# Optimization experiments

Measured on AMD Instinct MI355X. Metric: run time of the kernel, lower is better.

## Reference

```python
import jax, jax.numpy as jnp
import numpy as np

B, N, D, H, P, C, L = 2, 768, 512, 8, 64, 256, 6
NSEQ, NSP, NRD = 8, 8, 16
K = 2 * NSEQ + NSP + NRD  # 40 sparse neighbor slots
DH = D // H
LAT = 8


def _ln(x):
    m = jnp.mean(x, axis=-1, keepdims=True)
    v = jnp.var(x, axis=-1, keepdims=True)
    return (x - m) * jax.lax.rsqrt(v + 1e-5)


def _neighbors(ca, mask, rand_idx):
    # sequential neighbors: +-NSEQ offsets, clipped, with in-range validity
    offs = jnp.concatenate([jnp.arange(-NSEQ, 0), jnp.arange(1, NSEQ + 1)])
    base = jnp.arange(N)[:, None] + offs[None, :]                 # [N, 2*NSEQ]
    seq_idx = jnp.broadcast_to(jnp.clip(base, 0, N - 1)[None], (B, N, 2 * NSEQ))
    seq_in = jnp.broadcast_to(((base >= 0) & (base < N))[None], (B, N, 2 * NSEQ))
    # spatial KNN on CA coordinates (mask invalid residues and self)
    d2 = jnp.sum((ca[:, :, None, :] - ca[:, None, :, :]) ** 2, axis=-1)  # [B,N,N]
    big = jnp.float32(1e9)
    d2 = jnp.where(mask[:, None, :], d2, big)
    d2 = d2 + jnp.eye(N, dtype=d2.dtype) * big
    _, sp_idx = jax.lax.top_k(-d2, NSP)                            # [B,N,NSP]
    idx = jnp.concatenate([seq_idx.astype(jnp.int32), sp_idx.astype(jnp.int32),
                           rand_idx.astype(jnp.int32)], axis=-1)   # [B,N,K]
    b_ar = jnp.arange(B)[:, None, None]
    nb_mask = mask[b_ar, idx]                                      # neighbor validity
    extra = jnp.concatenate([seq_in, jnp.ones((B, N, NSP + NRD), bool)], axis=-1)
    valid = nb_mask & extra & mask[:, :, None]                     # [B,N,K]
    return idx, valid


def setup_inputs() -> dict:
    key = jax.random.key(0)
    ks = jax.random.split(key, 16)
    s = 0.02
    return {
        'seqs': jax.random.normal(ks[0], (B, N, D), jnp.float32),
        'cond': jax.random.normal(ks[1], (B, N, C), jnp.float32),
        'ca_coors': jax.random.normal(ks[2], (B, N, 3), jnp.float32) * 10.0,
        'pair_rep': jax.random.normal(ks[3], (B, N, N, P), jnp.float32),
        'mask': jnp.ones((B, N), bool),
        'rand_idx': jax.random.randint(ks[4], (B, N, NRD), 0, N, jnp.int32),
        'Wq': jax.random.normal(ks[5], (L, D, D), jnp.float32) * s,
        'Wk': jax.random.normal(ks[6], (L, D, D), jnp.float32) * s,
        'Wv': jax.random.normal(ks[7], (L, D, D), jnp.float32) * s,
        'Wo': jax.random.normal(ks[8], (L, D, D), jnp.float32) * s,
        'Wb': jax.random.normal(ks[9], (L, P, H), jnp.float32) * s,
        'Wc': jax.random.normal(ks[10], (L, C, 2 * D), jnp.float32) * s,
        'W1': jax.random.normal(ks[11], (L, D, 4 * D), jnp.float32) * s,
        'W2': jax.random.normal(ks[12], (L, 4 * D, D), jnp.float32) * s,
        'W_ca': jax.random.normal(ks[13], (D, 3), jnp.float32) * s,
        'W_lat': jax.random.normal(ks[14], (D, LAT), jnp.float32) * s,
    }


def reference(seqs, cond, ca_coors, pair_rep, mask, rand_idx,
              Wq, Wk, Wv, Wo, Wb, Wc, W1, W2, W_ca, W_lat):
    idx, valid = _neighbors(ca_coors, mask, rand_idx)              # [B,N,K]
    b_ar = jnp.arange(B)[:, None, None]
    # gather pair features once for all layers: [B,N,K,P]
    pair_g = jnp.take_along_axis(pair_rep, idx[:, :, :, None], axis=2)
    scale = 1.0 / jnp.sqrt(jnp.float32(DH))
    mview = mask[:, :, None].astype(seqs.dtype)
    x = seqs
    for l in range(L):
        h = _ln(x)
        ss = cond @ Wc[l]                                          # adaLN-style cond
        sc, sh = jnp.split(ss, 2, axis=-1)
        h = h * (1.0 + sc) + sh
        q = (h @ Wq[l]).reshape(B, N, H, DH)
        k_all = h @ Wk[l]
        v_all = h @ Wv[l]
        kg = k_all[b_ar, idx].reshape(B, N, K, H, DH)              # sparse gather
        vg = v_all[b_ar, idx].reshape(B, N, K, H, DH)
        q = _ln(q)                                                 # qk-layernorm
        kg = _ln(kg)
        bias = jnp.einsum('bnkp,ph->bhnk', pair_g, Wb[l])          # pair bias
        scores = jnp.einsum('bnhd,bnkhd->bhnk', q, kg) * scale + bias
        scores = jnp.where(valid[:, None, :, :], scores, -1e9)
        attn = jax.nn.softmax(scores, axis=-1)
        o = jnp.einsum('bhnk,bnkhd->bnhd', attn, vg).reshape(B, N, D)
        x = x + (o @ Wo[l]) * mview
        t = jax.nn.gelu(_ln(x) @ W1[l]) @ W2[l]                    # transition MLP
        x = x + t * mview
    hN = _ln(x)
    ca_out = hN @ W_ca                                             # [B,N,3]
    lat = hN @ W_lat                                               # [B,N,LAT]
    return jnp.concatenate([ca_out, lat], axis=-1)
```

## Files before the change

### kernel.cpp

```cpp
#include <hip/hip_runtime.h>
#include <hip/hip_bf16.h>


constexpr int B_  = 2;
constexpr int N_  = 768;
constexpr int D_  = 512;
constexpr int H_  = 8;
constexpr int P_  = 64;
constexpr int C_  = 256;
constexpr int L_  = 6;
constexpr int NSEQ = 8;
constexpr int NSP  = 8;
constexpr int NRD  = 16;
constexpr int K_   = 2 * NSEQ + NSP + NRD;
constexpr int DH_  = D_ / H_;
constexpr int BN_  = B_ * N_;
constexpr int D2_  = 2 * D_;
constexpr int D3_  = 3 * D_;
constexpr int D4_  = 4 * D_;

constexpr int FB_SS  = 0;
constexpr int FB_QKV = 512;
constexpr int FB_WO  = 2048;
constexpr int FB_W1  = 2560;
constexpr int FB_W2  = 4608;
constexpr int FB_TOT = 6656;

typedef __attribute__((ext_vector_type(8))) short bf16x8;
typedef __attribute__((ext_vector_type(4))) float floatx4;

__device__ __forceinline__ float waveRedSum(float v) {
#pragma unroll
    for (int o = 32; o > 0; o >>= 1) v += __shfl_xor(v, o, 64);
    return v;
}
__device__ __forceinline__ float waveRedMax(float v) {
#pragma unroll
    for (int o = 32; o > 0; o >>= 1) v = fmaxf(v, __shfl_xor(v, o, 64));
    return v;
}

__device__ __forceinline__ unsigned short bf_hi(float x) {
    unsigned u = __float_as_uint(x);
    return (unsigned short)((u + 0x7FFFu + ((u >> 16) & 1u)) >> 16);
}
__device__ __forceinline__ float bf_f(unsigned short h) {
    return __uint_as_float(((unsigned)h) << 16);
}
__device__ __forceinline__ void split2(float x0, float x1, unsigned& hp, unsigned& lp) {
    unsigned short h0 = bf_hi(x0), h1 = bf_hi(x1);
    unsigned short l0 = bf_hi(x0 - bf_f(h0)), l1 = bf_hi(x1 - bf_f(h1));
    hp = (unsigned)h0 | ((unsigned)h1 << 16);
    lp = (unsigned)l0 | ((unsigned)l1 << 16);
}

__device__ __forceinline__ float gelu_tanh(float x) {
    float u = x * x * x;
    float z = 0.7978845608028654f * (x + 0.044715f * u);
    float az = fabsf(z);
    float e = __expf(-2.f * az);
    float th = (1.f - e) / (1.f + e);
    th = (z < 0.f) ? -th : th;
    return 0.5f * x * (1.f + th);
}

__global__ void copy_kernel(const float4* __restrict__ in, float4* __restrict__ out, int n4) {
    int i = blockIdx.x * 256 + threadIdx.x;
    if (i < n4) out[i] = in[i];
}

__global__ __launch_bounds__(256) void knn_kernel(const float* __restrict__ ca,
                                                  const int* __restrict__ rnd,
                                                  int* __restrict__ idx) {
    __shared__ float sx[N_], sy[N_], sz[N_];
    __shared__ float cv[4];
    __shared__ int   ci[4];
    int bn = blockIdx.x;
    int b = bn / N_, n = bn % N_;
    int t = threadIdx.x;
    int wid = t >> 6, lane = t & 63;
    const float* cab = ca + (size_t)b * N_ * 3;
    for (int j = t; j < N_; j += 256) {
        sx[j] = cab[j * 3 + 0];
        sy[j] = cab[j * 3 + 1];
        sz[j] = cab[j * 3 + 2];
    }
    __syncthreads();
    float ax = sx[n], ay = sy[n], az = sz[n];

    float d2l[3];
    int   jls[3];
#pragma unroll
    for (int r = 0; r < 3; ++r) {
        int j = t + r * 256;
        float dx = ax - sx[j], dy = ay - sy[j], dz = az - sz[j];
        float d2 = dx * dx + dy * dy + dz * dz;
        if (j == n) d2 += 1e9f;
        d2l[r] = d2;
        jls[r] = j;
    }

    int base = bn * K_;
    if (t < 2 * NSEQ) {
        int off = (t < NSEQ) ? (t - NSEQ) : (t - NSEQ + 1);
        int p = n + off;
        p = p < 0 ? 0 : (p > N_ - 1 ? N_ - 1 : p);
        idx[base + t] = p;
    }
    if (t < NRD) idx[base + 2 * NSEQ + NSP + t] = rnd[bn * NRD + t];

    bool taken[3] = {false, false, false};
    for (int s = 0; s < NSP; ++s) {
        float bv = 3.4e38f;
        int   bi = N_;
#pragma unroll
        for (int r = 0; r < 3; ++r) {
            if (!taken[r]) {
                float v = d2l[r];
                if (v < bv || (v == bv && jls[r] < bi)) { bv = v; bi = jls[r]; }
            }
        }
#pragma unroll
        for (int o = 32; o > 0; o >>= 1) {
            float v2 = __shfl_xor(bv, o, 64);
            int   i2 = __shfl_xor(bi, o, 64);
            if (v2 < bv || (v2 == bv && i2 < bi)) { bv = v2; bi = i2; }
        }
        if (lane == 0) { cv[wid] = bv; ci[wid] = bi; }
        __syncthreads();
        float mv = cv[0]; int mi = ci[0];
#pragma unroll
        for (int w = 1; w < 4; ++w) {
            if (cv[w] < mv || (cv[w] == mv && ci[w] < mi)) { mv = cv[w]; mi = ci[w]; }
        }
        int sel = mi;
        if (t == 0) idx[base + 2 * NSEQ + s] = sel;
#pragma unroll
        for (int r = 0; r < 3; ++r)
            if (jls[r] == sel) taken[r] = true;
        __syncthreads();
    }
}

__global__ __launch_bounds__(256) void wconv_kernel(const float* __restrict__ Wc,
                                                    const float* __restrict__ Wq,
                                                    const float* __restrict__ Wk,
                                                    const float* __restrict__ Wv,
                                                    const float* __restrict__ Wo,
                                                    const float* __restrict__ W1,
                                                    const float* __restrict__ W2,
                                                    uint4* __restrict__ Wt, int l0) {
    int wid = threadIdx.x >> 6, lane = threadIdx.x & 63;
    int per = FB_TOT / 4;
    int slot = blockIdx.x / per;
    int l = l0 + slot;
    int fb = (blockIdx.x - slot * per) * 4 + wid;
    const float* src;
    int Nsrc, nsub, kstep;
    if (fb < FB_QKV) {
        int r = fb; nsub = r >> 3; kstep = r & 7;
        src = Wc + (size_t)l * C_ * D2_; Nsrc = D2_;
    } else if (fb < FB_WO) {
        int r = fb - FB_QKV; nsub = r >> 4; kstep = r & 15;
        int sel = nsub >> 5;
        const float* s0 = (sel == 0) ? Wq : ((sel == 1) ? Wk : Wv);
        src = s0 + (size_t)l * D_ * D_; Nsrc = D_; nsub &= 31;
    } else if (fb < FB_W1) {
        int r = fb - FB_WO; nsub = r >> 4; kstep = r & 15;
        src = Wo + (size_t)l * D_ * D_; Nsrc = D_;
    } else if (fb < FB_W2) {
        int r = fb - FB_W1; nsub = r >> 4; kstep = r & 15;
        src = W1 + (size_t)l * D_ * D4_; Nsrc = D4_;
    } else {
        int r = fb - FB_W2; nsub = r >> 6; kstep = r & 63;
        src = W2 + (size_t)l * D4_ * D_; Nsrc = D_;
    }
    int k0 = kstep * 32 + ((lane >> 4) << 3);
    int n = nsub * 16 + (lane & 15);
    unsigned hp[4], lp[4];
#pragma unroll
    for (int jj = 0; jj < 4; ++jj) {
        float x0 = src[(size_t)(k0 + 2 * jj) * Nsrc + n];
        float x1 = src[(size_t)(k0 + 2 * jj + 1) * Nsrc + n];
        split2(x0, x1, hp[jj], lp[jj]);
    }
    uint4* dst = Wt + ((size_t)slot * FB_TOT + fb) * 128;
    dst[lane]      = (uint4){hp[0], hp[1], hp[2], hp[3]};
    dst[64 + lane] = (uint4){lp[0], lp[1], lp[2], lp[3]};
}

__global__ __launch_bounds__(256) void pair_bias_kernel(const float* __restrict__ pair,
                                                        const float* __restrict__ WbL,
                                                        const int* __restrict__ idx,
                                                        float* __restrict__ biasL) {
    int wid = threadIdx.x >> 6, lane = threadIdx.x & 63;
    int t = blockIdx.x * 4 + wid;
    int bn = t / K_;
    int j = idx[t];
    float pv = pair[((size_t)bn * N_ + j) * P_ + lane];
    float4 wa = *(const float4*)&WbL[lane * 8];
    float4 wb = *(const float4*)&WbL[lane * 8 + 4];
    float r0 = waveRedSum(pv * wa.x);
    float r1 = waveRedSum(pv * wa.y);
    float r2 = waveRedSum(pv * wa.z);
    float r3 = waveRedSum(pv * wa.w);
    float r4 = waveRedSum(pv * wb.x);
    float r5 = waveRedSum(pv * wb.y);
    float r6 = waveRedSum(pv * wb.z);
    float r7 = waveRedSum(pv * wb.w);
    float res = r0;
    res = (lane == 1) ? r1 : res;
    res = (lane == 2) ? r2 : res;
    res = (lane == 3) ? r3 : res;
    res = (lane == 4) ? r4 : res;
    res = (lane == 5) ? r5 : res;
    res = (lane == 6) ? r6 : res;
    res = (lane == 7) ? r7 : res;
    if (lane < 8) biasL[(size_t)t * 8 + lane] = res;
}

#define STAGE_A(BUF)                                                        \
    {                                                                       \
        unsigned h0, h1, h2, h3, p0, p1, p2, p3;                            \
        split2(fa0.x, fa0.y, h0, p0); split2(fa0.z, fa0.w, h1, p1);         \
        split2(fa1.x, fa1.y, h2, p2); split2(fa1.z, fa1.w, h3, p3);         \
        As[BUF][sidx]      = (uint4){h0, h1, h2, h3};                       \
        As[BUF][64 + sidx] = (uint4){p0, p1, p2, p3};                       \
    }

#define MFMA_PHASE(BUF, BH, BL)                                             \
    {                                                                       \
        bf16x8 Ah[4], Al[4];                                                \
        _Pragma("unroll")                                                   \
        for (int mf = 0; mf < 4; ++mf) {                                    \
            Ah[mf] = *(const bf16x8*)&As[BUF][mf * 128 + lane];             \
            Al[mf] = *(const bf16x8*)&As[BUF][mf * 128 + 64 + lane];        \
        }                                                                   \
        _Pragma("unroll")                                                   \
        for (int mf = 0; mf < 4; ++mf) {                                    \
            _Pragma("unroll")                                               \
            for (int nf = 0; nf < 2; ++nf) {                                \
                acc[mf][nf] = __builtin_amdgcn_mfma_f32_16x16x32_bf16(      \
                    Ah[mf], BH[nf], acc[mf][nf], 0, 0, 0);                  \
                acc[mf][nf] = __builtin_amdgcn_mfma_f32_16x16x32_bf16(      \
                    Ah[mf], BL[nf], acc[mf][nf], 0, 0, 0);                  \
                acc[mf][nf] = __builtin_amdgcn_mfma_f32_16x16x32_bf16(      \
                    Al[mf], BH[nf], acc[mf][nf], 0, 0, 0);                  \
            }                                                               \
        }                                                                   \
    }

template <int GELU, int RES>
__global__ __launch_bounds__(256, 2) void gemm_mfma(const float* __restrict__ A,
                                                    const uint4* __restrict__ WtB,
                                                    const float* __restrict__ Cres,
                                                    float* __restrict__ Cout,
                                                    int M, int Nout, int Kd) {
    __shared__ uint4 As[2][512];
    int tid = threadIdx.x;
    int wid = tid >> 6, lane = tid & 63;
    int m0 = blockIdx.y * 64, n0 = blockIdx.x * 128;
    int kd32 = Kd >> 5;

    int sr = tid >> 2, soct = tid & 3;
    const float* Ap = A + (size_t)(m0 + sr) * Kd + soct * 8;
    int sidx = (sr >> 4) * 128 + (sr & 15) + soct * 16;

    int nsub0 = (n0 >> 4) + wid * 2;
    const uint4* Bp0 = WtB + (size_t)nsub0 * kd32 * 128 + lane;
    const uint4* Bp1 = WtB + (size_t)(nsub0 + 1) * kd32 * 128 + lane;

    floatx4 acc[4][2];
#pragma unroll
    for (int i = 0; i < 4; ++i)
#pragma unroll
        for (int j = 0; j < 2; ++j) acc[i][j] = (floatx4){0.f, 0.f, 0.f, 0.f};

    float4 fa0, fa1;
    bf16x8 BhA[2], BlA[2], BhB[2], BlB[2];

    fa0 = *(const float4*)(Ap);
    fa1 = *(const float4*)(Ap + 4);
    STAGE_A(0)
    BhA[0] = *(const bf16x8*)(Bp0);
    BlA[0] = *(const bf16x8*)(Bp0 + 64);
    BhA[1] = *(const bf16x8*)(Bp1);
    BlA[1] = *(const bf16x8*)(Bp1 + 64);
    __syncthreads();

    for (int ks = 0; ks < kd32; ks += 2) {
        fa0 = *(const float4*)(Ap + (ks + 1) * 32);
        fa1 = *(const float4*)(Ap + (ks + 1) * 32 + 4);
        BhB[0] = *(const bf16x8*)(Bp0 + (size_t)(ks + 1) * 128);
        BlB[0] = *(const bf16x8*)(Bp0 + (size_t)(ks + 1) * 128 + 64);
        BhB[1] = *(const bf16x8*)(Bp1 + (size_t)(ks + 1) * 128);
        BlB[1] = *(const bf16x8*)(Bp1 + (size_t)(ks + 1) * 128 + 64);
        MFMA_PHASE(0, BhA, BlA)
        STAGE_A(1)
        __syncthreads();

        bool more = (ks + 2) < kd32;
        if (more) {
            fa0 = *(const float4*)(Ap + (ks + 2) * 32);
            fa1 = *(const float4*)(Ap + (ks + 2) * 32 + 4);
            BhA[0] = *(const bf16x8*)(Bp0 + (size_t)(ks + 2) * 128);
            BlA[0] = *(const bf16x8*)(Bp0 + (size_t)(ks + 2) * 128 + 64);
            BhA[1] = *(const bf16x8*)(Bp1 + (size_t)(ks + 2) * 128);
            BlA[1] = *(const bf16x8*)(Bp1 + (size_t)(ks + 2) * 128 + 64);
        }
        MFMA_PHASE(1, BhB, BlB)
        if (more) STAGE_A(0)
        __syncthreads();
    }

    int r0 = (lane >> 4) << 2;
    int cc = lane & 15;
#pragma unroll
    for (int mf = 0; mf < 4; ++mf) {
#pragma unroll
        for (int nf = 0; nf < 2; ++nf) {
            int nn = n0 + (wid * 2 + nf) * 16 + cc;
#pragma unroll
            for (int r = 0; r < 4; ++r) {
                int mm = m0 + mf * 16 + r0 + r;
                float x = acc[mf][nf][r];
                if (GELU) x = gelu_tanh(x);
                if (RES) x += Cres[(size_t)mm * Nout + nn];
                Cout[(size_t)mm * Nout + nn] = x;
            }
        }
    }
}

template <bool MOD>
__global__ __launch_bounds__(256) void ln_kernel(const float* __restrict__ x,
                                                 const float* __restrict__ ss,
                                                 float* __restrict__ out) {
    __shared__ float sred[8];
    int row = blockIdx.x, t = threadIdx.x;
    int wid = t >> 6, lane = t & 63;
    const float* xr = x + (size_t)row * D_;
    float v0 = xr[t], v1 = xr[t + 256];
    float p = waveRedSum(v0 + v1);
    float q = waveRedSum(v0 * v0 + v1 * v1);
    if (lane == 0) { sred[wid] = p; sred[wid + 4] = q; }
    __syncthreads();
    float mean = (sred[0] + sred[1] + sred[2] + sred[3]) * (1.0f / D_);
    float var = (sred[4] + sred[5] + sred[6] + sred[7]) * (1.0f / D_) - mean * mean;
    float rs = rsqrtf(var + 1e-5f);
    float h0 = (v0 - mean) * rs;
    float h1 = (v1 - mean) * rs;
    if (MOD) {
        const float* ssr = ss + (size_t)row * D2_;
        h0 = h0 * (1.f + ssr[t]) + ssr[t + D_];
        h1 = h1 * (1.f + ssr[t + 256]) + ssr[t + 256 + D_];
    }
    float* orow = out + (size_t)row * D_;
    orow[t] = h0;
    orow[t + 256] = h1;
}

__global__ __launch_bounds__(256) void ln_head_kernel(float* __restrict__ qkv) {
    int wid = threadIdx.x >> 6, lane = threadIdx.x & 63;
    int vec = blockIdx.x * 4 + wid;
    int part = vec / (BN_ * H_);
    int rem = vec - part * (BN_ * H_);
    int r = rem / H_, h = rem - r * H_;
    float* p = qkv + (size_t)r * D3_ + part * D_ + h * DH_;
    float v = p[lane];
    float s = waveRedSum(v);
    float sq = waveRedSum(v * v);
    float m = s * (1.f / DH_);
    float var = sq * (1.f / DH_) - m * m;
    p[lane] = (v - m) * rsqrtf(var + 1e-5f);
}

__global__ __launch_bounds__(256) void attn_kernel(const float* __restrict__ qkv,
                                                   const int* __restrict__ idx,
                                                   const float* __restrict__ biasL,
                                                   float* __restrict__ o) {
    int wid = threadIdx.x >> 6, lane = threadIdx.x & 63;
    int g = blockIdx.x * 4 + wid;
    int h = g & 7;
    int bn = g >> 3;
    int n = bn % N_;
    int bnb = bn - n;

    int myj = 0;
    float mybias = 0.f;
    bool myvalid = false;
    if (lane < K_) {
        myj = idx[bn * K_ + lane];
        mybias = biasL[((size_t)bn * K_ + lane) * H_ + h];
        myvalid = true;
        if (lane < 2 * NSEQ) {
            int off = (lane < NSEQ) ? (lane - NSEQ) : (lane - NSEQ + 1);
            int p = n + off;
            myvalid = (p >= 0) && (p < N_);
        }
    }
    float qv = qkv[(size_t)bn * D3_ + h * DH_ + lane];
    float sc = -1e9f;
#pragma unroll 8
    for (int k = 0; k < K_; ++k) {
        int j = __shfl(myj, k);
        float kv = qkv[(size_t)(bnb + j) * D3_ + D_ + h * DH_ + lane];
        float dot = waveRedSum(qv * kv);
        if (lane == k) sc = myvalid ? (dot * 0.125f + mybias) : -1e9f;
    }
    float mx = waveRedMax(lane < K_ ? sc : -3.4e38f);
    float e = (lane < K_) ? expf(sc - mx) : 0.f;
    float den = waveRedSum(e);
    float w = e / den;
    float acc = 0.f;
#pragma unroll 8
    for (int k = 0; k < K_; ++k) {
        int j = __shfl(myj, k);
        float wk = __shfl(w, k);
        acc += wk * qkv[(size_t)(bnb + j) * D3_ + 2 * D_ + h * DH_ + lane];
    }
    o[(size_t)bn * D_ + h * DH_ + lane] = acc;
}

__global__ __launch_bounds__(256) void final_kernel(const float* __restrict__ x,
                                                    const float* __restrict__ Wca,
                                                    const float* __restrict__ Wlat,
                                                    float* __restrict__ out) {
    __shared__ float sred[8];
    __shared__ float hn[D_];
    int row = blockIdx.x, t = threadIdx.x;
    int wid = t >> 6, lane = t & 63;
    const float* xr = x + (size_t)row * D_;
    float v0 = xr[t], v1 = xr[t + 256];
    float p = waveRedSum(v0 + v1);
    float q = waveRedSum(v0 * v0 + v1 * v1);
    if (lane == 0) { sred[wid] = p; sred[wid + 4] = q; }
    __syncthreads();
    float mean = (sred[0] + sred[1] + sred[2] + sred[3]) * (1.0f / D_);
    float var = (sred[4] + sred[5] + sred[6] + sred[7]) * (1.0f / D_) - mean * mean;
    float rs = rsqrtf(var + 1e-5f);
    hn[t] = (v0 - mean) * rs;
    hn[t + 256] = (v1 - mean) * rs;
    __syncthreads();
    for (int c = wid; c < 11; c += 4) {
        float s = 0.f;
#pragma unroll
        for (int u = 0; u < 8; ++u) {
            int d = lane + u * 64;
            float w = (c < 3) ? Wca[d * 3 + c] : Wlat[d * 8 + (c - 3)];
            s += hn[d] * w;
        }
        s = waveRedSum(s);
        if (lane == 0) out[(size_t)row * 11 + c] = s;
    }
}

extern "C" void kernel_launch(void* const* d_in, const int* in_sizes, int n_in,
                              void* d_out, int out_size, void* d_ws, size_t ws_size,
                              hipStream_t stream) {
    const float* seqs = (const float*)d_in[0];
    const float* cond = (const float*)d_in[1];
    const float* ca   = (const float*)d_in[2];
    const float* pair = (const float*)d_in[3];
    const int*   rnd  = (const int*)d_in[5];
    const float* Wq   = (const float*)d_in[6];
    const float* Wk   = (const float*)d_in[7];
    const float* Wv   = (const float*)d_in[8];
    const float* Wo   = (const float*)d_in[9];
    const float* Wb   = (const float*)d_in[10];
    const float* Wc   = (const float*)d_in[11];
    const float* W1   = (const float*)d_in[12];
    const float* W2   = (const float*)d_in[13];
    const float* Wca  = (const float*)d_in[14];
    const float* Wlat = (const float*)d_in[15];
    float* out = (float*)d_out;

    const size_t wtSlotF = (size_t)FB_TOT * 512;
    const size_t fixedF = (size_t)BN_ * D_ * 3 + (size_t)BN_ * K_ * H_ + BN_ * K_
                        + (size_t)BN_ * D2_ + (size_t)BN_ * D3_;
    bool allW = ws_size >= (fixedF + (size_t)L_ * wtSlotF) * 4;
    int nslots = allW ? L_ : 1;

    float* ws = (float*)d_ws;
    float* x     = ws;  ws += BN_ * D_;
    float* hbuf  = ws;  ws += BN_ * D_;
    float* obuf  = ws;  ws += BN_ * D_;
    float* biasL = ws;  ws += BN_ * K_ * H_;
    int*   idx   = (int*)ws;  ws += BN_ * K_;
    uint4* Wt    = (uint4*)ws; ws += nslots * wtSlotF;
    float* ss    = ws;  ws += BN_ * D2_;
    float* qkv   = ws;  ws += BN_ * D3_;
    float* t1    = ss;

    copy_kernel<<<BN_ * D_ / 4 / 256, 256, 0, stream>>>((const float4*)seqs, (float4*)x, BN_ * D_ / 4);
    knn_kernel<<<BN_, 256, 0, stream>>>(ca, rnd, idx);
    if (allW)
        wconv_kernel<<<L_ * (FB_TOT / 4), 256, 0, stream>>>(Wc, Wq, Wk, Wv, Wo, W1, W2, Wt, 0);

    dim3 blk(256);
    for (int l = 0; l < L_; ++l) {
        if (!allW)
            wconv_kernel<<<FB_TOT / 4, 256, 0, stream>>>(Wc, Wq, Wk, Wv, Wo, W1, W2, Wt, l);
        const uint4* WtL = Wt + (size_t)(allW ? l : 0) * FB_TOT * 128;
        const float* WbL = Wb + (size_t)l * P_ * H_;

        pair_bias_kernel<<<BN_ * K_ / 4, blk, 0, stream>>>(pair, WbL, idx, biasL);
        gemm_mfma<0, 0><<<dim3(D2_ / 128, BN_ / 64), blk, 0, stream>>>(
            cond, WtL + (size_t)FB_SS * 128, nullptr, ss, BN_, D2_, C_);
        ln_kernel<true><<<BN_, blk, 0, stream>>>(x, ss, hbuf);
        gemm_mfma<0, 0><<<dim3(D3_ / 128, BN_ / 64), blk, 0, stream>>>(
            hbuf, WtL + (size_t)FB_QKV * 128, nullptr, qkv, BN_, D3_, D_);
        ln_head_kernel<<<BN_ * H_ * 2 / 4, blk, 0, stream>>>(qkv);
        attn_kernel<<<BN_ * H_ / 4, blk, 0, stream>>>(qkv, idx, biasL, obuf);
        gemm_mfma<0, 1><<<dim3(D_ / 128, BN_ / 64), blk, 0, stream>>>(
            obuf, WtL + (size_t)FB_WO * 128, x, x, BN_, D_, D_);
        ln_kernel<false><<<BN_, blk, 0, stream>>>(x, nullptr, hbuf);
        gemm_mfma<1, 0><<<dim3(D4_ / 128, BN_ / 64), blk, 0, stream>>>(
            hbuf, WtL + (size_t)FB_W1 * 128, nullptr, t1, BN_, D4_, D_);
        gemm_mfma<0, 1><<<dim3(D_ / 128, BN_ / 64), blk, 0, stream>>>(
            t1, WtL + (size_t)FB_W2 * 128, x, x, BN_, D_, D4_);
    }

    final_kernel<<<BN_, blk, 0, stream>>>(x, Wca, Wlat, out);
}
```

Measured before the change: 1.747 ms.

## Split-K residual GEMMs with atomics, fuse LN into W1 GEMM, hoist pair bias

Pair-bias computation for all layers is hoisted into one launch before the layer loop, so each gathered pair row is read once instead of once per layer. The Wo and W2 GEMMs are split two ways along K and accumulate into x with atomicAdd. This doubles their block count and replaces the explicit residual read. The plain LayerNorm before W1 becomes a small stats kernel, and normalization is applied while staging A tiles inside the GEMM, removing the hbuf write and read. GEMM blocks are also remapped with a swizzled 1D grid. Atomic accumulation makes the float summation order nondeterministic, and the full path needs more workspace.

```diff
diff --git a/kernel.cpp b/kernel.cpp
--- a/kernel.cpp
+++ b/kernel.cpp
@@ -18,6 +18,7 @@
 constexpr int D2_  = 2 * D_;
 constexpr int D3_  = 3 * D_;
 constexpr int D4_  = 4 * D_;
+constexpr int MROWS_ = BN_ / 64;
 
 constexpr int FB_SS  = 0;
 constexpr int FB_QKV = 512;
@@ -190,40 +191,69 @@
 }
 
 __global__ __launch_bounds__(256) void pair_bias_kernel(const float* __restrict__ pair,
-                                                        const float* __restrict__ WbL,
+                                                        const float* __restrict__ Wb,
                                                         const int* __restrict__ idx,
-                                                        float* __restrict__ biasL) {
+                                                        float* __restrict__ biasAll,
+                                                        int l0, int nl) {
     int wid = threadIdx.x >> 6, lane = threadIdx.x & 63;
     int t = blockIdx.x * 4 + wid;
     int bn = t / K_;
     int j = idx[t];
     float pv = pair[((size_t)bn * N_ + j) * P_ + lane];
-    float4 wa = *(const float4*)&WbL[lane * 8];
-    float4 wb = *(const float4*)&WbL[lane * 8 + 4];
-    float r0 = waveRedSum(pv * wa.x);
-    float r1 = waveRedSum(pv * wa.y);
-    float r2 = waveRedSum(pv * wa.z);
-    float r3 = waveRedSum(pv * wa.w);
-    float r4 = waveRedSum(pv * wb.x);
-    float r5 = waveRedSum(pv * wb.y);
-    float r6 = waveRedSum(pv * wb.z);
-    float r7 = waveRedSum(pv * wb.w);
-    float res = r0;
-    res = (lane == 1) ? r1 : res;
-    res = (lane == 2) ? r2 : res;
-    res = (lane == 3) ? r3 : res;
-    res = (lane == 4) ? r4 : res;
-    res = (lane == 5) ? r5 : res;
-    res = (lane == 6) ? r6 : res;
-    res = (lane == 7) ? r7 : res;
-    if (lane < 8) biasL[(size_t)t * 8 + lane] = res;
+    for (int ll = 0; ll < nl; ++ll) {
+        const float* WbL = Wb + (size_t)(l0 + ll) * P_ * H_;
+        float4 wa = *(const float4*)&WbL[lane * 8];
+        float4 wb = *(const float4*)&WbL[lane * 8 + 4];
+        float r0 = waveRedSum(pv * wa.x);
+        float r1 = waveRedSum(pv * wa.y);
+        float r2 = waveRedSum(pv * wa.z);
+        float r3 = waveRedSum(pv * wa.w);
+        float r4 = waveRedSum(pv * wb.x);
+        float r5 = waveRedSum(pv * wb.y);
+        float r6 = waveRedSum(pv * wb.z);
+        float r7 = waveRedSum(pv * wb.w);
+        float res = r0;
+        res = (lane == 1) ? r1 : res;
+        res = (lane == 2) ? r2 : res;
+        res = (lane == 3) ? r3 : res;
+        res = (lane == 4) ? r4 : res;
+        res = (lane == 5) ? r5 : res;
+        res = (lane == 6) ? r6 : res;
+        res = (lane == 7) ? r7 : res;
+        if (lane < 8) biasAll[((size_t)ll * BN_ * K_ + t) * 8 + lane] = res;
+    }
+}
+
+__global__ __launch_bounds__(256) void ln_stats_kernel(const float* __restrict__ x,
+                                                       float2* __restrict__ lnst) {
+    int wid = threadIdx.x >> 6, lane = threadIdx.x & 63;
+    int row = blockIdx.x * 4 + wid;
+    const float4* xr4 = (const float4*)(x + (size_t)row * D_);
+    float4 a = xr4[lane];
+    float4 b = xr4[64 + lane];
+    float s = waveRedSum(a.x + a.y + a.z + a.w + b.x + b.y + b.z + b.w);
+    float q = waveRedSum(a.x * a.x + a.y * a.y + a.z * a.z + a.w * a.w +
+                         b.x * b.x + b.y * b.y + b.z * b.z + b.w * b.w);
+    if (lane == 0) {
+        float mean = s * (1.0f / D_);
+        float var = q * (1.0f / D_) - mean * mean;
+        lnst[row] = (float2){mean, rsqrtf(var + 1e-5f)};
+    }
 }
 
 #define STAGE_A(BUF)                                                        \
     {                                                                       \
+        float a0 = fa0.x, a1 = fa0.y, a2 = fa0.z, a3 = fa0.w;               \
+        float a4 = fa1.x, a5 = fa1.y, a6 = fa1.z, a7 = fa1.w;               \
+        if (LNMODE == 1) {                                                  \
+            a0 = (a0 - mu) * rsg; a1 = (a1 - mu) * rsg;                     \
+            a2 = (a2 - mu) * rsg; a3 = (a3 - mu) * rsg;                     \
+            a4 = (a4 - mu) * rsg; a5 = (a5 - mu) * rsg;                     \
+            a6 = (a6 - mu) * rsg; a7 = (a7 - mu) * rsg;                     \
+        }                                                                   \
         unsigned h0, h1, h2, h3, p0, p1, p2, p3;                            \
-        split2(fa0.x, fa0.y, h0, p0); split2(fa0.z, fa0.w, h1, p1);         \
-        split2(fa1.x, fa1.y, h2, p2); split2(fa1.z, fa1.w, h3, p3);         \
+        split2(a0, a1, h0, p0); split2(a2, a3, h1, p1);                     \
+        split2(a4, a5, h2, p2); split2(a6, a7, h3, p3);                     \
         As[BUF][sidx]      = (uint4){h0, h1, h2, h3};                       \
         As[BUF][64 + sidx] = (uint4){p0, p1, p2, p3};                       \
     }
@@ -250,25 +280,43 @@
         }                                                                   \
     }
 
-template <int GELU, int RES>
+template <int GELU, int RES, int LNMODE, int KSPLIT>
 __global__ __launch_bounds__(256, 2) void gemm_mfma(const float* __restrict__ A,
                                                     const uint4* __restrict__ WtB,
+                                                    const float2* __restrict__ lnst,
                                                     const float* __restrict__ Cres,
                                                     float* __restrict__ Cout,
-                                                    int M, int Nout, int Kd) {
+                                                    int Nout, int Kd, int nblkC) {
     __shared__ uint4 As[2][512];
     int tid = threadIdx.x;
     int wid = tid >> 6, lane = tid & 63;
-    int m0 = blockIdx.y * 64, n0 = blockIdx.x * 128;
-    int kd32 = Kd >> 5;
+
+    int sid = blockIdx.x;
+    int total0 = nblkC * MROWS_;
+    int split = sid / total0;
+    int id = sid - split * total0;
+    int P = total0 >> 3;
+    int L = (id & 7) * P + (id >> 3);
+    int bcol = L / MROWS_, brow = L - bcol * MROWS_;
+    int m0 = brow * 64, n0 = bcol * 128;
+
+    int kd32t = Kd >> 5;
+    int kdsp = kd32t / KSPLIT;
+    int ks0 = split * kdsp;
 
     int sr = tid >> 2, soct = tid & 3;
-    const float* Ap = A + (size_t)(m0 + sr) * Kd + soct * 8;
+    const float* Ap = A + (size_t)(m0 + sr) * Kd + ks0 * 32 + soct * 8;
     int sidx = (sr >> 4) * 128 + (sr & 15) + soct * 16;
 
+    float mu = 0.f, rsg = 1.f;
+    if (LNMODE == 1) {
+        float2 st = lnst[m0 + sr];
+        mu = st.x; rsg = st.y;
+    }
+
     int nsub0 = (n0 >> 4) + wid * 2;
-    const uint4* Bp0 = WtB + (size_t)nsub0 * kd32 * 128 + lane;
-    const uint4* Bp1 = WtB + (size_t)(nsub0 + 1) * kd32 * 128 + lane;
+    const uint4* Bp0 = WtB + ((size_t)nsub0 * kd32t + ks0) * 128 + lane;
+    const uint4* Bp1 = WtB + ((size_t)(nsub0 + 1) * kd32t + ks0) * 128 + lane;
 
     floatx4 acc[4][2];
 #pragma unroll
@@ -288,7 +336,7 @@
     BlA[1] = *(const bf16x8*)(Bp1 + 64);
     __syncthreads();
 
-    for (int ks = 0; ks < kd32; ks += 2) {
+    for (int ks = 0; ks < kdsp; ks += 2) {
         fa0 = *(const float4*)(Ap + (ks + 1) * 32);
         fa1 = *(const float4*)(Ap + (ks + 1) * 32 + 4);
         BhB[0] = *(const bf16x8*)(Bp0 + (size_t)(ks + 1) * 128);
@@ -299,7 +347,7 @@
         STAGE_A(1)
         __syncthreads();
 
-        bool more = (ks + 2) < kd32;
+        bool more = (ks + 2) < kdsp;
         if (more) {
             fa0 = *(const float4*)(Ap + (ks + 2) * 32);
             fa1 = *(const float4*)(Ap + (ks + 2) * 32 + 4);
@@ -325,17 +373,20 @@
                 int mm = m0 + mf * 16 + r0 + r;
                 float x = acc[mf][nf][r];
                 if (GELU) x = gelu_tanh(x);
-                if (RES) x += Cres[(size_t)mm * Nout + nn];
-                Cout[(size_t)mm * Nout + nn] = x;
+                if (RES == 1) x += Cres[(size_t)mm * Nout + nn];
+                if (RES == 2) {
+                    atomicAdd(&Cout[(size_t)mm * Nout + nn], x);
+                } else {
+                    Cout[(size_t)mm * Nout + nn] = x;
+                }
             }
         }
     }
 }
 
-template <bool MOD>
-__global__ __launch_bounds__(256) void ln_kernel(const float* __restrict__ x,
-                                                 const float* __restrict__ ss,
-                                                 float* __restrict__ out) {
+__global__ __launch_bounds__(256) void ln_mod_kernel(const float* __restrict__ x,
+                                                     const float* __restrict__ ss,
+                                                     float* __restrict__ out) {
     __shared__ float sred[8];
     int row = blockIdx.x, t = threadIdx.x;
     int wid = t >> 6, lane = t & 63;
@@ -350,11 +401,9 @@
     float rs = rsqrtf(var + 1e-5f);
     float h0 = (v0 - mean) * rs;
     float h1 = (v1 - mean) * rs;
-    if (MOD) {
-        const float* ssr = ss + (size_t)row * D2_;
-        h0 = h0 * (1.f + ssr[t]) + ssr[t + D_];
-        h1 = h1 * (1.f + ssr[t + 256]) + ssr[t + 256 + D_];
-    }
+    const float* ssr = ss + (size_t)row * D2_;
+    h0 = h0 * (1.f + ssr[t]) + ssr[t + D_];
+    h1 = h1 * (1.f + ssr[t + 256]) + ssr[t + 256 + D_];
     float* orow = out + (size_t)row * D_;
     orow[t] = h0;
     orow[t + 256] = h1;
@@ -476,49 +525,54 @@
     float* out = (float*)d_out;
 
     const size_t wtSlotF = (size_t)FB_TOT * 512;
-    const size_t fixedF = (size_t)BN_ * D_ * 3 + (size_t)BN_ * K_ * H_ + BN_ * K_
-                        + (size_t)BN_ * D2_ + (size_t)BN_ * D3_;
-    bool allW = ws_size >= (fixedF + (size_t)L_ * wtSlotF) * 4;
-    int nslots = allW ? L_ : 1;
+    const size_t biasSlotF = (size_t)BN_ * K_ * H_;
+    const size_t needFull = (3ULL * BN_ * D_ + (size_t)L_ * biasSlotF + BN_ * K_ + 2 * BN_
+                             + (size_t)L_ * wtSlotF + BN_ * D2_ + BN_ * D3_) * 4;
+    bool full = ws_size >= needFull;
+    int nW = full ? L_ : 1, nB = full ? L_ : 1;
 
     float* ws = (float*)d_ws;
-    float* x     = ws;  ws += BN_ * D_;
-    float* hbuf  = ws;  ws += BN_ * D_;
-    float* obuf  = ws;  ws += BN_ * D_;
-    float* biasL = ws;  ws += BN_ * K_ * H_;
-    int*   idx   = (int*)ws;  ws += BN_ * K_;
-    uint4* Wt    = (uint4*)ws; ws += nslots * wtSlotF;
-    float* ss    = ws;  ws += BN_ * D2_;
-    float* qkv   = ws;  ws += BN_ * D3_;
-    float* t1    = ss;
+    float* x       = ws;  ws += BN_ * D_;
+    float* hbuf    = ws;  ws += BN_ * D_;
+    float* obuf    = ws;  ws += BN_ * D_;
+    float* biasAll = ws;  ws += (size_t)nB * biasSlotF;
+    int*   idx     = (int*)ws;  ws += BN_ * K_;
+    float2* lnst   = (float2*)ws;  ws += 2 * BN_;
+    uint4* Wt      = (uint4*)ws; ws += (size_t)nW * wtSlotF;
+    float* ss      = ws;  ws += BN_ * D2_;
+    float* qkv     = ws;  ws += BN_ * D3_;
+    float* t1      = ss;
 
     copy_kernel<<<BN_ * D_ / 4 / 256, 256, 0, stream>>>((const float4*)seqs, (float4*)x, BN_ * D_ / 4);
     knn_kernel<<<BN_, 256, 0, stream>>>(ca, rnd, idx);
-    if (allW)
+    if (full) {
         wconv_kernel<<<L_ * (FB_TOT / 4), 256, 0, stream>>>(Wc, Wq, Wk, Wv, Wo, W1, W2, Wt, 0);
+        pair_bias_kernel<<<BN_ * K_ / 4, 256, 0, stream>>>(pair, Wb, idx, biasAll, 0, L_);
+    }
 
     dim3 blk(256);
     for (int l = 0; l < L_; ++l) {
-        if (!allW)
+        if (!full) {
             wconv_kernel<<<FB_TOT / 4, 256, 0, stream>>>(Wc, Wq, Wk, Wv, Wo, W1, W2, Wt, l);
-        const uint4* WtL = Wt + (size_t)(allW ? l : 0) * FB_TOT * 128;
-        const float* WbL = Wb + (size_t)l * P_ * H_;
-
-        pair_bias_kernel<<<BN_ * K_ / 4, blk, 0, stream>>>(pair, WbL, idx, biasL);
-        gemm_mfma<0, 0><<<dim3(D2_ / 128, BN_ / 64), blk, 0, stream>>>(
-            cond, WtL + (size_t)FB_SS * 128, nullptr, ss, BN_, D2_, C_);
-        ln_kernel<true><<<BN_, blk, 0, stream>>>(x, ss, hbuf);
-        gemm_mfma<0, 0><<<dim3(D3_ / 128, BN_ / 64), blk, 0, stream>>>(
-            hbuf, WtL + (size_t)FB_QKV * 128, nullptr, qkv, BN_, D3_, D_);
+            pair_bias_kernel<<<BN_ * K_ / 4, 256, 0, stream>>>(pair, Wb, idx, biasAll, l, 1);
+        }
+        const uint4* WtL = Wt + (size_t)(full ? l : 0) * FB_TOT * 128;
+        const float* biasL = biasAll + (size_t)(full ? l : 0) * biasSlotF;
+
+        gemm_mfma<0, 0, 0, 1><<<8 * MROWS_, blk, 0, stream>>>(
+            cond, WtL + (size_t)FB_SS * 128, nullptr, nullptr, ss, D2_, C_, 8);
+        ln_mod_kernel<<<BN_, blk, 0, stream>>>(x, ss, hbuf);
+        gemm_mfma<0, 0, 0, 1><<<12 * MROWS_, blk, 0, stream>>>(
+            hbuf, WtL + (size_t)FB_QKV * 128, nullptr, nullptr, qkv, D3_, D_, 12);
         ln_head_kernel<<<BN_ * H_ * 2 / 4, blk, 0, stream>>>(qkv);
         attn_kernel<<<BN_ * H_ / 4, blk, 0, stream>>>(qkv, idx, biasL, obuf);
-        gemm_mfma<0, 1><<<dim3(D_ / 128, BN_ / 64), blk, 0, stream>>>(
-            obuf, WtL + (size_t)FB_WO * 128, x, x, BN_, D_, D_);
-        ln_kernel<false><<<BN_, blk, 0, stream>>>(x, nullptr, hbuf);
-        gemm_mfma<1, 0><<<dim3(D4_ / 128, BN_ / 64), blk, 0, stream>>>(
-            hbuf, WtL + (size_t)FB_W1 * 128, nullptr, t1, BN_, D4_, D_);
-        gemm_mfma<0, 1><<<dim3(D_ / 128, BN_ / 64), blk, 0, stream>>>(
-            t1, WtL + (size_t)FB_W2 * 128, x, x, BN_, D_, D4_);
+        gemm_mfma<0, 2, 0, 2><<<4 * MROWS_ * 2, blk, 0, stream>>>(
+            obuf, WtL + (size_t)FB_WO * 128, nullptr, nullptr, x, D_, D_, 4);
+        ln_stats_kernel<<<BN_ / 4, blk, 0, stream>>>(x, lnst);
+        gemm_mfma<1, 0, 1, 1><<<16 * MROWS_, blk, 0, stream>>>(
+            x, WtL + (size_t)FB_W1 * 128, lnst, nullptr, t1, D4_, D_, 16);
+        gemm_mfma<0, 2, 0, 2><<<4 * MROWS_ * 2, blk, 0, stream>>>(
+            t1, WtL + (size_t)FB_W2 * 128, nullptr, nullptr, x, D_, D4_, 4);
     }
 
     final_kernel<<<BN_, blk, 0, stream>>>(x, Wca, Wlat, out);
```

After: 1.572 ms. 1.11x faster.
